# Kernel tuning notes

Measured on AMD Instinct MI355X. Metric: run time of the kernel, lower is better.

## Reference

```python
import jax, jax.numpy as jnp
import numpy as np

N, H, W, C = 2048, 64, 64, 8
E, G, M = 4, 512, 512            # experts, group size per class, max_output_cells
CELLS = [128, 256, 384, 512]     # classes_config.values()


def setup_inputs() -> dict:
    key = jax.random.key(0)
    k = jax.random.split(key, 6)
    inputs = jax.random.normal(k[0], (N, H, W, C), dtype=jnp.float32)
    # input_config: class -> sample indices (equal partition of the batch)
    indices = jnp.arange(N, dtype=jnp.int32).reshape(E, G)
    W1 = jax.random.normal(k[1], (E, 1, 1, C, C), dtype=jnp.float32) * 0.1
    W3 = jax.random.normal(k[2], (E, 3, 3, C, C), dtype=jnp.float32) * 0.1
    Wskip = jax.random.normal(k[3], (E, 1, 1, C, 2 * C), dtype=jnp.float32) * 0.1
    Wd = jax.random.normal(k[4], (E, 2 * C, M), dtype=jnp.float32) * 0.1
    # zero-pad each expert's output beyond its num_output_layer_cells
    cell_mask = (jnp.arange(M)[None, :] < jnp.asarray(CELLS)[:, None]).astype(jnp.float32)
    return {"inputs": inputs, "indices": indices, "W1": W1, "W3": W3,
            "Wskip": Wskip, "Wd": Wd, "cell_mask": cell_mask}


def _conv(x, w):
    # x: [G,H,W,Cin], w: [kh,kw,Cin,Cout] -> [G,H,W,Cout], SAME padding
    return jax.lax.conv_general_dilated(x, w, (1, 1), 'SAME',
                                        dimension_numbers=('NHWC', 'HWIO', 'NHWC'))


def _expert(x, w1, w3, ws, wd, mask):
    # Hybrid inception + skip: parallel 1x1/3x3 branches, channel concat, 1x1-projected skip
    b1 = jax.nn.relu(_conv(x, w1))           # [G,H,W,C]
    b2 = jax.nn.relu(_conv(x, w3))           # [G,H,W,C]
    y = jnp.concatenate([b1, b2], axis=-1) + _conv(x, ws)  # [G,H,W,2C]
    pooled = y.mean(axis=(1, 2))             # [G,2C]
    return (pooled @ wd) * mask[None, :]     # [G,M], padded to max_output_cells


def reference(inputs, indices, W1, W3, Wskip, Wd, cell_mask):
    # class-indexed gather: [E,G,H,W,C]
    groups = inputs[indices]
    # dispatch each group to its expert, vmapped over experts
    outs = jax.vmap(_expert)(groups, W1, W3, Wskip, Wd, cell_mask)  # [E,G,M]
    # concat along batch in class order (matches outputs.extend + tf.concat axis=0)
    return outs.reshape(E * G, M)
```

## Files before the change

### kernel.cpp

```cpp
#include <hip/hip_runtime.h>
#include <hip/hip_bf16.h>

#define MM 512

typedef short bf16x8 __attribute__((ext_vector_type(8)));
typedef float f32x4  __attribute__((ext_vector_type(4)));

static __device__ inline short f2bf(float f) {
    __hip_bfloat16 h = __float2bfloat16(f);
    return *reinterpret_cast<short*>(&h);
}

__global__ __launch_bounds__(256, 4)
void conv_moe_mfma(const float* __restrict__ x,
                   const int*   __restrict__ idx,
                   const float* __restrict__ W1,
                   const float* __restrict__ W3,
                   const float* __restrict__ Wsk,
                   const float* __restrict__ Wd,
                   const float* __restrict__ cmask,
                   float*       __restrict__ out)
{
    __shared__ short xbf[2][18][66][8];
    __shared__ float red[4][16];
    __shared__ float redx[4][8];
    __shared__ float rsum[16];
    __shared__ float rsumx[8];
    __shared__ float pooledS[16];

    const int b    = blockIdx.x;
    const int e    = b >> 9;
    const int tid  = threadIdx.x;
    const int lane = tid & 63;
    const int wid  = tid >> 6;
    const int g    = lane >> 4;
    const int p    = lane & 15;
    const int CB   = wid << 4;

    const int samp = idx[b];
    const float* xb = x + (size_t)samp * 32768;

    const float* w3 = W3 + e * 576;
    const float* w1 = W1 + e * 64;
    bf16x8 bf0, bf1, bf2, bid;
    #pragma unroll
    for (int j = 0; j < 8; ++j) {
        float v0 = 0.f, v1 = 0.f, v2 = 0.f, vi = 0.f;
        if (p >= 8) {
            v0 = w3[g * 64 + j * 8 + (p - 8)];
            v1 = w3[(4 + g) * 64 + j * 8 + (p - 8)];
            if (g == 0) v2 = w3[8 * 64 + j * 8 + (p - 8)];
        } else {
            if (g == 0) { v1 = w1[j * 8 + p]; vi = (j == p) ? 1.f : 0.f; }
        }
        bf0[j] = f2bf(v0); bf1[j] = f2bf(v1); bf2[j] = f2bf(v2); bid[j] = f2bf(vi);
    }

    int off0, off1, off2;
    { const int t = g;     const int dr = t / 3, dc = t % 3; off0 = (dr * 66 + CB + p + dc) * 8; }
    { const int t = 4 + g; const int dr = t / 3, dc = t % 3; off1 = (dr * 66 + CB + p + dc) * 8; }
    {                      const int dr = 2,     dc = 2;     off2 = (dr * 66 + CB + p + dc) * 8; }

    if (tid < 72) {
        const int bb = tid & 1, t = tid >> 1;
        const int rr = t % 18, side = t / 18;
        bf16x8 zv = {0,0,0,0,0,0,0,0};
        *(bf16x8*)&xbf[bb][rr][side ? 65 : 0][0] = zv;
    }

    #define STAGE(S, BB)                                                        \
    {                                                                           \
        const int r0s = (S) * 16;                                               \
        _Pragma("unroll")                                                       \
        for (int j5 = 0; j5 < 5; ++j5) {                                        \
            const int j = j5 * 256 + tid;                                       \
            if (j < 1152) {                                                     \
                const int lrow = j >> 6, c = j & 63;                            \
                const int r = r0s - 1 + lrow;                                   \
                bf16x8 v = {0,0,0,0,0,0,0,0};                                   \
                if (r >= 0 && r < 64) {                                         \
                    const float4* s4 = (const float4*)(xb + (((r << 6) + c) << 3)); \
                    const float4 aa = s4[0], bb4 = s4[1];                        \
                    v[0]=f2bf(aa.x); v[1]=f2bf(aa.y); v[2]=f2bf(aa.z); v[3]=f2bf(aa.w); \
                    v[4]=f2bf(bb4.x); v[5]=f2bf(bb4.y); v[6]=f2bf(bb4.z); v[7]=f2bf(bb4.w); \
                }                                                               \
                *(bf16x8*)&xbf[BB][lrow][c + 1][0] = v;                         \
            }                                                                   \
        }                                                                       \
    }

    f32x4 ssum = {0.f, 0.f, 0.f, 0.f};
    f32x4 acc2 = {0.f, 0.f, 0.f, 0.f};

    STAGE(0, 0);
    __syncthreads();

    #pragma unroll 1
    for (int s = 0; s < 4; ++s) {
        if (s == 0) STAGE(1, 1);
        if (s == 1) STAGE(2, 0);
        if (s == 2) STAGE(3, 1);

        const short* base = &xbf[s & 1][0][0][0];
        #pragma unroll 2
        for (int rl = 0; rl < 16; ++rl) {
            const short* rbase = base + rl * (66 * 8);
            const bf16x8 a0 = *(const bf16x8*)(rbase + off0);
            const bf16x8 a1 = *(const bf16x8*)(rbase + off1);
            const bf16x8 a2 = *(const bf16x8*)(rbase + off2);
            f32x4 d = {0.f, 0.f, 0.f, 0.f};
            d = __builtin_amdgcn_mfma_f32_16x16x32_bf16(a0, bf0, d, 0, 0, 0);
            d = __builtin_amdgcn_mfma_f32_16x16x32_bf16(a1, bf1, d, 0, 0, 0);
            d = __builtin_amdgcn_mfma_f32_16x16x32_bf16(a2, bf2, d, 0, 0, 0);
            acc2 = __builtin_amdgcn_mfma_f32_16x16x32_bf16(a1, bid, acc2, 0, 0, 0);
            ssum[0] += fmaxf(d[0], 0.f);
            ssum[1] += fmaxf(d[1], 0.f);
            ssum[2] += fmaxf(d[2], 0.f);
            ssum[3] += fmaxf(d[3], 0.f);
        }
        __syncthreads();
    }

    float scon = ssum[0] + ssum[1] + ssum[2] + ssum[3];
    float sxs  = acc2[0] + acc2[1] + acc2[2] + acc2[3];
    scon += __shfl_xor(scon, 16);
    scon += __shfl_xor(scon, 32);
    sxs  += __shfl_xor(sxs, 16);
    sxs  += __shfl_xor(sxs, 32);
    if (lane < 16) red[wid][lane]  = scon;
    if (lane < 8)  redx[wid][lane] = sxs;
    __syncthreads();
    if (tid < 16) rsum[tid]  = (red[0][tid] + red[1][tid] + red[2][tid] + red[3][tid]) * (1.f / 4096.f);
    if (tid < 8)  rsumx[tid] = (redx[0][tid] + redx[1][tid] + redx[2][tid] + redx[3][tid]) * (1.f / 4096.f);
    __syncthreads();

    if (tid < 16) {
        float acc = rsum[tid];
        #pragma unroll
        for (int ci = 0; ci < 8; ++ci)
            acc += rsumx[ci] * Wsk[e * 128 + ci * 16 + tid];
        pooledS[tid] = acc;
    }
    __syncthreads();

    const float* wd = Wd + (size_t)e * 16 * MM;
    const float* cm = cmask + e * MM;
    #pragma unroll 1
    for (int m = tid; m < MM; m += 256) {
        float acc = 0.f;
        #pragma unroll
        for (int k = 0; k < 16; ++k) acc += pooledS[k] * wd[k * MM + m];
        out[(size_t)b * MM + m] = acc * cm[m];
    }
}

extern "C" void kernel_launch(void* const* d_in, const int* in_sizes, int n_in,
                              void* d_out, int out_size, void* d_ws, size_t ws_size,
                              hipStream_t stream) {
    const float* x    = (const float*)d_in[0];
    const int*   idx  = (const int*)  d_in[1];
    const float* W1   = (const float*)d_in[2];
    const float* W3   = (const float*)d_in[3];
    const float* Wsk  = (const float*)d_in[4];
    const float* Wd   = (const float*)d_in[5];
    const float* cmsk = (const float*)d_in[6];
    float* out = (float*)d_out;

    conv_moe_mfma<<<2048, 256, 0, stream>>>(x, idx, W1, W3, Wsk, Wd, cmsk, out);
}
```

Baseline: 61.18 us.

## Replace LDS double buffer with register prefetch of next input stage

Removes the double-buffered LDS tile and uses a single LDS buffer. The next 16-row stage is loaded into registers (prefetch) while MFMA work runs on the current stage, then converted to bf16 and written to LDS at the start of the next iteration. This halves LDS usage, which may raise occupancy, and lets the global loads overlap with compute. It costs about 40 extra VGPRs per thread, which under launch_bounds(256,4) could cause spilling or lower occupancy.

```diff
diff --git a/kernel.cpp b/kernel.cpp
--- a/kernel.cpp
+++ b/kernel.cpp
@@ -21,7 +21,7 @@
                    const float* __restrict__ cmask,
                    float*       __restrict__ out)
 {
-    __shared__ short xbf[2][18][66][8];
+    __shared__ short xbf[18][66][8];
     __shared__ float red[4][16];
     __shared__ float redx[4][8];
     __shared__ float rsum[16];
@@ -61,30 +61,47 @@
     { const int t = 4 + g; const int dr = t / 3, dc = t % 3; off1 = (dr * 66 + CB + p + dc) * 8; }
     {                      const int dr = 2,     dc = 2;     off2 = (dr * 66 + CB + p + dc) * 8; }
 
-    if (tid < 72) {
-        const int bb = tid & 1, t = tid >> 1;
-        const int rr = t % 18, side = t / 18;
+    if (tid < 36) {
+        const int rr = tid % 18, side = tid / 18;
         bf16x8 zv = {0,0,0,0,0,0,0,0};
-        *(bf16x8*)&xbf[bb][rr][side ? 65 : 0][0] = zv;
+        *(bf16x8*)&xbf[rr][side ? 65 : 0][0] = zv;
     }
 
-    #define STAGE(S, BB)                                                        \
+    const float4 z4 = make_float4(0.f, 0.f, 0.f, 0.f);
+    float4 ra[5][2];
+
+    #define STAGE_LOAD(S)                                                       \
     {                                                                           \
         const int r0s = (S) * 16;                                               \
         _Pragma("unroll")                                                       \
         for (int j5 = 0; j5 < 5; ++j5) {                                        \
             const int j = j5 * 256 + tid;                                       \
+            ra[j5][0] = z4; ra[j5][1] = z4;                                     \
             if (j < 1152) {                                                     \
                 const int lrow = j >> 6, c = j & 63;                            \
                 const int r = r0s - 1 + lrow;                                   \
-                bf16x8 v = {0,0,0,0,0,0,0,0};                                   \
                 if (r >= 0 && r < 64) {                                         \
                     const float4* s4 = (const float4*)(xb + (((r << 6) + c) << 3)); \
-                    const float4 aa = s4[0], bb4 = s4[1];                        \
-                    v[0]=f2bf(aa.x); v[1]=f2bf(aa.y); v[2]=f2bf(aa.z); v[3]=f2bf(aa.w); \
-                    v[4]=f2bf(bb4.x); v[5]=f2bf(bb4.y); v[6]=f2bf(bb4.z); v[7]=f2bf(bb4.w); \
+                    ra[j5][0] = s4[0];                                          \
+                    ra[j5][1] = s4[1];                                          \
                 }                                                               \
-                *(bf16x8*)&xbf[BB][lrow][c + 1][0] = v;                         \
+            }                                                                   \
+        }                                                                       \
+    }
+
+    #define STAGE_WRITE()                                                       \
+    {                                                                           \
+        _Pragma("unroll")                                                       \
+        for (int j5 = 0; j5 < 5; ++j5) {                                        \
+            const int j = j5 * 256 + tid;                                       \
+            if (j < 1152) {                                                     \
+                const int lrow = j >> 6, c = j & 63;                            \
+                bf16x8 v;                                                       \
+                v[0] = f2bf(ra[j5][0].x); v[1] = f2bf(ra[j5][0].y);             \
+                v[2] = f2bf(ra[j5][0].z); v[3] = f2bf(ra[j5][0].w);             \
+                v[4] = f2bf(ra[j5][1].x); v[5] = f2bf(ra[j5][1].y);             \
+                v[6] = f2bf(ra[j5][1].z); v[7] = f2bf(ra[j5][1].w);             \
+                *(bf16x8*)&xbf[lrow][c + 1][0] = v;                             \
             }                                                                   \
         }                                                                       \
     }
@@ -92,16 +109,15 @@
     f32x4 ssum = {0.f, 0.f, 0.f, 0.f};
     f32x4 acc2 = {0.f, 0.f, 0.f, 0.f};
 
-    STAGE(0, 0);
-    __syncthreads();
+    STAGE_LOAD(0);
 
     #pragma unroll 1
     for (int s = 0; s < 4; ++s) {
-        if (s == 0) STAGE(1, 1);
-        if (s == 1) STAGE(2, 0);
-        if (s == 2) STAGE(3, 1);
+        STAGE_WRITE();
+        __syncthreads();
+        if (s < 3) STAGE_LOAD(s + 1);
 
-        const short* base = &xbf[s & 1][0][0][0];
+        const short* base = &xbf[0][0][0];
         #pragma unroll 2
         for (int rl = 0; rl < 16; ++rl) {
             const short* rbase = base + rl * (66 * 8);
```

After: 52.29 us. 14.5% less time.

## Use circular row buffer with register-prefetched loads overlapping MFMA compute

Applied to the files above, without the earlier changes.

Replaces the double-buffered 18-row LDS tiles with a single 36-row circular buffer, so only 16 new rows are loaded per stage instead of re-staging the halo rows. Global loads for the next stage are issued into registers before the MFMA loop and converted and written to LDS afterwards, letting memory latency overlap compute. It also skips the third A-operand LDS load for lanes whose weights are zero. The cost is extra registers for the prefetch buffer, modular index arithmetic in the inner loop, and a possible occupancy drop.

```diff
diff --git a/kernel.cpp b/kernel.cpp
--- a/kernel.cpp
+++ b/kernel.cpp
@@ -1,7 +1,9 @@
 #include <hip/hip_runtime.h>
 #include <hip/hip_bf16.h>
 
-#define MM 512
+#define MM    512
+#define NROWS 36
+#define ROWSZ (66 * 8)
 
 typedef short bf16x8 __attribute__((ext_vector_type(8)));
 typedef float f32x4  __attribute__((ext_vector_type(4)));
@@ -21,7 +23,7 @@
                    const float* __restrict__ cmask,
                    float*       __restrict__ out)
 {
-    __shared__ short xbf[2][18][66][8];
+    __shared__ short xbf[NROWS][66][8];
     __shared__ float red[4][16];
     __shared__ float redx[4][8];
     __shared__ float rsum[16];
@@ -56,69 +58,115 @@
         bf0[j] = f2bf(v0); bf1[j] = f2bf(v1); bf2[j] = f2bf(v2); bid[j] = f2bf(vi);
     }
 
-    int off0, off1, off2;
-    { const int t = g;     const int dr = t / 3, dc = t % 3; off0 = (dr * 66 + CB + p + dc) * 8; }
-    { const int t = 4 + g; const int dr = t / 3, dc = t % 3; off1 = (dr * 66 + CB + p + dc) * 8; }
-    {                      const int dr = 2,     dc = 2;     off2 = (dr * 66 + CB + p + dc) * 8; }
+    const int d0 = g / 3;
+    const int d1 = (4 + g) / 3;
+    const int c0 = (CB + p + (g % 3)) * 8;
+    const int c1 = (CB + p + ((4 + g) % 3)) * 8;
+    const int c2 = (CB + p + 2) * 8;
 
     if (tid < 72) {
-        const int bb = tid & 1, t = tid >> 1;
-        const int rr = t % 18, side = t / 18;
+        const int rr = tid >> 1, side = tid & 1;
         bf16x8 zv = {0,0,0,0,0,0,0,0};
-        *(bf16x8*)&xbf[bb][rr][side ? 65 : 0][0] = zv;
-    }
-
-    #define STAGE(S, BB)                                                        \
-    {                                                                           \
-        const int r0s = (S) * 16;                                               \
-        _Pragma("unroll")                                                       \
-        for (int j5 = 0; j5 < 5; ++j5) {                                        \
-            const int j = j5 * 256 + tid;                                       \
-            if (j < 1152) {                                                     \
-                const int lrow = j >> 6, c = j & 63;                            \
-                const int r = r0s - 1 + lrow;                                   \
-                bf16x8 v = {0,0,0,0,0,0,0,0};                                   \
-                if (r >= 0 && r < 64) {                                         \
-                    const float4* s4 = (const float4*)(xb + (((r << 6) + c) << 3)); \
-                    const float4 aa = s4[0], bb4 = s4[1];                        \
-                    v[0]=f2bf(aa.x); v[1]=f2bf(aa.y); v[2]=f2bf(aa.z); v[3]=f2bf(aa.w); \
-                    v[4]=f2bf(bb4.x); v[5]=f2bf(bb4.y); v[6]=f2bf(bb4.z); v[7]=f2bf(bb4.w); \
-                }                                                               \
-                *(bf16x8*)&xbf[BB][lrow][c + 1][0] = v;                         \
-            }                                                                   \
-        }                                                                       \
-    }
+        *(bf16x8*)&xbf[rr][side ? 65 : 0][0] = zv;
+    }
+
+    const float4 z4 = make_float4(0.f, 0.f, 0.f, 0.f);
+    float4 ra[5][2];
+
+    #pragma unroll
+    for (int j5 = 0; j5 < 5; ++j5) {
+        const int j = j5 * 256 + tid;
+        ra[j5][0] = z4; ra[j5][1] = z4;
+        if (j < 1152) {
+            const int lrow = j >> 6, c = j & 63;
+            const int r = lrow - 1;
+            if (r >= 0) {
+                const float4* s4 = (const float4*)(xb + (((r << 6) + c) << 3));
+                ra[j5][0] = s4[0];
+                ra[j5][1] = s4[1];
+            }
+        }
+    }
+    #pragma unroll
+    for (int j5 = 0; j5 < 5; ++j5) {
+        const int j = j5 * 256 + tid;
+        if (j < 1152) {
+            const int lrow = j >> 6, c = j & 63;
+            bf16x8 v;
+            v[0] = f2bf(ra[j5][0].x); v[1] = f2bf(ra[j5][0].y);
+            v[2] = f2bf(ra[j5][0].z); v[3] = f2bf(ra[j5][0].w);
+            v[4] = f2bf(ra[j5][1].x); v[5] = f2bf(ra[j5][1].y);
+            v[6] = f2bf(ra[j5][1].z); v[7] = f2bf(ra[j5][1].w);
+            *(bf16x8*)&xbf[lrow][c + 1][0] = v;
+        }
+    }
+    __syncthreads();
 
     f32x4 ssum = {0.f, 0.f, 0.f, 0.f};
     f32x4 acc2 = {0.f, 0.f, 0.f, 0.f};
 
-    STAGE(0, 0);
-    __syncthreads();
-
     #pragma unroll 1
     for (int s = 0; s < 4; ++s) {
-        if (s == 0) STAGE(1, 1);
-        if (s == 1) STAGE(2, 0);
-        if (s == 2) STAGE(3, 1);
-
-        const short* base = &xbf[s & 1][0][0][0];
-        #pragma unroll 2
-        for (int rl = 0; rl < 16; ++rl) {
-            const short* rbase = base + rl * (66 * 8);
-            const bf16x8 a0 = *(const bf16x8*)(rbase + off0);
-            const bf16x8 a1 = *(const bf16x8*)(rbase + off1);
-            const bf16x8 a2 = *(const bf16x8*)(rbase + off2);
-            f32x4 d = {0.f, 0.f, 0.f, 0.f};
-            d = __builtin_amdgcn_mfma_f32_16x16x32_bf16(a0, bf0, d, 0, 0, 0);
-            d = __builtin_amdgcn_mfma_f32_16x16x32_bf16(a1, bf1, d, 0, 0, 0);
-            d = __builtin_amdgcn_mfma_f32_16x16x32_bf16(a2, bf2, d, 0, 0, 0);
-            acc2 = __builtin_amdgcn_mfma_f32_16x16x32_bf16(a1, bid, acc2, 0, 0, 0);
-            ssum[0] += fmaxf(d[0], 0.f);
-            ssum[1] += fmaxf(d[1], 0.f);
-            ssum[2] += fmaxf(d[2], 0.f);
-            ssum[3] += fmaxf(d[3], 0.f);
-        }
-        __syncthreads();
+        if (s < 3) {
+            const int rbase = 16 * s + 17;
+            #pragma unroll
+            for (int j5 = 0; j5 < 4; ++j5) {
+                const int j = j5 * 256 + tid;
+                const int lrow = j >> 6, c = j & 63;
+                const int r = rbase + lrow;
+                ra[j5][0] = z4; ra[j5][1] = z4;
+                if (r < 64) {
+                    const float4* s4 = (const float4*)(xb + (((r << 6) + c) << 3));
+                    ra[j5][0] = s4[0];
+                    ra[j5][1] = s4[1];
+                }
+            }
+        }
+
+        {
+            int tb = 16 * s;
+            const int sbase = (tb >= NROWS) ? tb - NROWS : tb;
+            const short* base = &xbf[0][0][0];
+            #pragma unroll 2
+            for (int rl = 0; rl < 16; ++rl) {
+                const int srl = sbase + rl;
+                int t0 = srl + d0; t0 = (t0 >= NROWS) ? t0 - NROWS : t0;
+                int t1 = srl + d1; t1 = (t1 >= NROWS) ? t1 - NROWS : t1;
+                int t2 = srl + 2;  t2 = (t2 >= NROWS) ? t2 - NROWS : t2;
+                const bf16x8 a0 = *(const bf16x8*)(base + t0 * ROWSZ + c0);
+                const bf16x8 a1 = *(const bf16x8*)(base + t1 * ROWSZ + c1);
+                bf16x8 a2 = {0,0,0,0,0,0,0,0};
+                if (g == 0)
+                    a2 = *(const bf16x8*)(base + t2 * ROWSZ + c2);
+                f32x4 d = {0.f, 0.f, 0.f, 0.f};
+                d = __builtin_amdgcn_mfma_f32_16x16x32_bf16(a0, bf0, d, 0, 0, 0);
+                d = __builtin_amdgcn_mfma_f32_16x16x32_bf16(a1, bf1, d, 0, 0, 0);
+                d = __builtin_amdgcn_mfma_f32_16x16x32_bf16(a2, bf2, d, 0, 0, 0);
+                acc2 = __builtin_amdgcn_mfma_f32_16x16x32_bf16(a1, bid, acc2, 0, 0, 0);
+                ssum[0] += fmaxf(d[0], 0.f);
+                ssum[1] += fmaxf(d[1], 0.f);
+                ssum[2] += fmaxf(d[2], 0.f);
+                ssum[3] += fmaxf(d[3], 0.f);
+            }
+        }
+
+        if (s < 3) {
+            int wt = 16 * s + 18;
+            const int wbase = (wt >= NROWS) ? wt - NROWS : wt;
+            #pragma unroll
+            for (int j5 = 0; j5 < 4; ++j5) {
+                const int j = j5 * 256 + tid;
+                const int lrow = j >> 6, c = j & 63;
+                int ws = wbase + lrow; ws = (ws >= NROWS) ? ws - NROWS : ws;
+                bf16x8 v;
+                v[0] = f2bf(ra[j5][0].x); v[1] = f2bf(ra[j5][0].y);
+                v[2] = f2bf(ra[j5][0].z); v[3] = f2bf(ra[j5][0].w);
+                v[4] = f2bf(ra[j5][1].x); v[5] = f2bf(ra[j5][1].y);
+                v[6] = f2bf(ra[j5][1].z); v[7] = f2bf(ra[j5][1].w);
+                *(bf16x8*)&xbf[ws][c + 1][0] = v;
+            }
+            __syncthreads();
+        }
     }
 
     float scon = ssum[0] + ssum[1] + ssum[2] + ssum[3];
```

Measured after the change: 57.56 us. 1.06x faster.
